# Optimization experiments

Hardware: AMD Instinct MI355X
Metric: run time of the kernel (lower is better)

## Reference

```python
import jax, jax.numpy as jnp
import numpy as np

B, N, E, DJ, DE = 1024, 400, 128, 128, 128  # batch, nodes, edges, joint dim, edge dim (E must equal DJ and DE for BatchNorm1d on 3D input)
BN_EPS = 1e-5


def setup_inputs() -> dict:
    key = jax.random.key(0)
    ks = jax.random.split(key, 8)
    gout = jax.random.normal(ks[0], (B, N, DJ), dtype=jnp.float32)
    eout = jax.random.normal(ks[1], (B, E, DE), dtype=jnp.float32)
    start_shift = jax.random.uniform(ks[2], (B, E, N), dtype=jnp.float32)
    end_shift = jax.random.uniform(ks[3], (B, E, N), dtype=jnp.float32)
    # Linear params: nn.init.normal_(std=0.001), bias 0
    W1 = 0.001 * jax.random.normal(ks[4], (DJ, 2 * DJ), dtype=jnp.float32)
    b1 = jnp.zeros((DJ,), dtype=jnp.float32)
    W2 = 0.001 * jax.random.normal(ks[5], (DE, DJ), dtype=jnp.float32)
    b2 = jnp.zeros((DE,), dtype=jnp.float32)
    # BatchNorm affine params: weight=1, bias=0
    g1 = jnp.ones((DJ,), dtype=jnp.float32)
    beta1 = jnp.zeros((DJ,), dtype=jnp.float32)
    g2 = jnp.ones((DE,), dtype=jnp.float32)
    beta2 = jnp.zeros((DE,), dtype=jnp.float32)
    return {"gout": gout, "eout": eout, "start_shift": start_shift, "end_shift": end_shift,
            "W1": W1, "b1": b1, "W2": W2, "b2": b2,
            "g1": g1, "beta1": beta1, "g2": g2, "beta2": beta2}


def batchnorm1d(x, gamma, beta):
    # PyTorch BatchNorm1d on 3D input: channels at dim 1, biased variance over dims (0, 2)
    mean = jnp.mean(x, axis=(0, 2), keepdims=True)
    var = jnp.mean(jnp.square(x - mean), axis=(0, 2), keepdims=True)
    xhat = (x - mean) * jax.lax.rsqrt(var + BN_EPS)
    return xhat * gamma[None, :, None] + beta[None, :, None]


def reference(gout, eout, start_shift, end_shift, W1, b1, W2, b2, g1, beta1, g2, beta2):
    # node -> edge gather via dense shift matmuls: [B,E,N] @ [B,N,DJ] -> [B,E,DJ]
    start_nodes = jnp.matmul(start_shift, gout)
    end_nodes = jnp.matmul(end_shift, gout)
    x = jnp.concatenate([start_nodes, end_nodes], axis=2)  # [B, E, 2*DJ]
    h = jnp.einsum('bef,df->bed', x, W1) + b1  # Linear(2*DJ -> DJ)
    h = jax.nn.relu(batchnorm1d(h, g1, beta1))
    h = jnp.einsum('bed,od->beo', h, W2) + b2  # Linear(DJ -> DE)
    res = batchnorm1d(h, g2, beta2)
    return jax.nn.relu(eout + res)
```

## Files before the change

### kernel.cpp

```cpp
#include <hip/hip_runtime.h>
#include <stdint.h>

#define BB 1024
#define NN 400
#define EE 128
#define DD 128
#define NSLOT 64
#define GTS 424
#define NKP 212

typedef float f32x4 __attribute__((ext_vector_type(4)));
typedef short bf16x8 __attribute__((ext_vector_type(8)));
typedef short bf16x4 __attribute__((ext_vector_type(4)));

__device__ __forceinline__ short f2bf(float f) {
    uint32_t u = __builtin_bit_cast(uint32_t, f);
    u += 0x7fffu + ((u >> 16) & 1u);
    return (short)(u >> 16);
}

__device__ __forceinline__ float bf2f(short s) {
    return __builtin_bit_cast(float, (uint32_t)((uint16_t)s) << 16);
}

__device__ __forceinline__ bf16x8 cvt8(const f32x4 a, const f32x4 b) {
    bf16x8 r;
    r[0] = f2bf(a[0]); r[1] = f2bf(a[1]); r[2] = f2bf(a[2]); r[3] = f2bf(a[3]);
    r[4] = f2bf(b[0]); r[5] = f2bf(b[1]); r[6] = f2bf(b[2]); r[7] = f2bf(b[3]);
    return r;
}

__global__ __launch_bounds__(1024, 1)
void k1_gemm(const float* __restrict__ gout, const float* __restrict__ ss,
             const float* __restrict__ es, const float* __restrict__ W1,
             const float* __restrict__ b1, unsigned short* __restrict__ h,
             float* __restrict__ stats1)
{
    __shared__ short lds[66560];
    short* GT  = lds;
    short* Ps  = lds;
    short* W1s = lds + 32768;

    const int b   = blockIdx.x;
    const int t   = threadIdx.x;
    const int w   = t >> 6;
    const int l   = t & 63;
    const int l15 = l & 15;
    const int l4  = l >> 4;

    {
        const int d   = t & 127;
        const int kpb = t >> 7;
        const float* gb = gout + (size_t)b * NN * DD + d;
        for (int kp = kpb; kp < NKP; kp += 8) {
            int k = 2 * kp;
            float v0 = 0.f, v1 = 0.f;
            if (k < NN) { v0 = gb[(size_t)k * DD]; v1 = gb[(size_t)(k + 1) * DD]; }
            uint32_t pk = (uint32_t)(uint16_t)f2bf(v0) |
                          ((uint32_t)(uint16_t)f2bf(v1) << 16);
            *(uint32_t*)&GT[d * GTS + 2 * kp] = pk;
        }
    }
    __syncthreads();

    const int arow = (w & 7) * 16 + l15;
    const float* abase = ((w < 8) ? ss : es) + ((size_t)b * EE + arow) * NN;

    f32x4 acc[8];
#pragma unroll
    for (int cf = 0; cf < 8; ++cf) acc[cf] = f32x4{0.f, 0.f, 0.f, 0.f};

    auto ld_a = [&](int k0) -> bf16x8 {
        int kk = k0 + l4 * 8;
        f32x4 x0{0.f, 0.f, 0.f, 0.f}, x1{0.f, 0.f, 0.f, 0.f};
        if (kk < NN) { x0 = *(const f32x4*)(abase + kk); x1 = *(const f32x4*)(abase + kk + 4); }
        return cvt8(x0, x1);
    };

    bf16x8 a_cur = ld_a(0);
    const int NK = 13;
    for (int s = 0; s < NK; ++s) {
        bf16x8 a_nxt = a_cur;
        if (s + 1 < NK) a_nxt = ld_a((s + 1) * 32);
        const int k0 = s * 32;
#pragma unroll
        for (int cf = 0; cf < 8; ++cf) {
            bf16x8 gf = *(const bf16x8*)&GT[(cf * 16 + l15) * GTS + k0 + l4 * 8];
            acc[cf] = __builtin_amdgcn_mfma_f32_16x16x32_bf16(a_cur, gf, acc[cf], 0, 0, 0);
        }
        a_cur = a_nxt;
    }
    __syncthreads();

#pragma unroll
    for (int cf = 0; cf < 8; ++cf)
#pragma unroll
        for (int r = 0; r < 4; ++r) {
            int row = w * 16 + l4 * 4 + r;
            int col = cf * 16 + l15;
            Ps[row * 128 + (((col >> 3) ^ (row & 7)) << 3) + (col & 7)] = f2bf(acc[cf][r]);
        }
    {
        const int j  = t >> 3;
        const int kc = t & 7;
        const float* wp = W1 + (size_t)j * 256 + kc * 32;
        short* dst = &W1s[j * 264 + kc * 32];
#pragma unroll
        for (int i = 0; i < 4; ++i) {
            f32x4 x0 = *(const f32x4*)(wp + i * 8);
            f32x4 x1 = *(const f32x4*)(wp + i * 8 + 4);
            *(bf16x8*)(dst + i * 8) = cvt8(x0, x1);
        }
    }
    __syncthreads();

    const int mt = w >> 1;
    const int jh = w & 1;
    f32x4 acc2[4];
#pragma unroll
    for (int cf = 0; cf < 4; ++cf) acc2[cf] = f32x4{0.f, 0.f, 0.f, 0.f};

#pragma unroll
    for (int kf = 0; kf < 8; ++kf) {
        int roff = (kf >= 4) ? 128 : 0;
        int kcol = (kf & 3) * 32 + l4 * 8;
        int row  = roff + mt * 16 + l15;
        int cb   = kcol >> 3;
        bf16x8 xf = *(const bf16x8*)&Ps[row * 128 + ((cb ^ (row & 7)) << 3)];
#pragma unroll
        for (int cf = 0; cf < 4; ++cf) {
            int j = jh * 64 + cf * 16 + l15;
            bf16x8 wf = *(const bf16x8*)&W1s[j * 264 + kf * 32 + l4 * 8];
            acc2[cf] = __builtin_amdgcn_mfma_f32_16x16x32_bf16(xf, wf, acc2[cf], 0, 0, 0);
        }
    }
    __syncthreads();

    float* red = (float*)lds;
    float s_r[4] = {0.f, 0.f, 0.f, 0.f};
    float q_r[4] = {0.f, 0.f, 0.f, 0.f};
#pragma unroll
    for (int cf = 0; cf < 4; ++cf) {
        float bv = b1[jh * 64 + cf * 16 + l15];
        f32x4 v = acc2[cf] + bv;
#pragma unroll
        for (int r = 0; r < 4; ++r) {
            int e = mt * 16 + l4 * 4 + r;
            h[((size_t)b * EE + e) * DD + jh * 64 + cf * 16 + l15] = (unsigned short)f2bf(v[r]);
            s_r[r] += v[r];
            q_r[r] += v[r] * v[r];
        }
    }
#pragma unroll
    for (int r = 0; r < 4; ++r) {
        float s = s_r[r], q = q_r[r];
        s += __shfl_xor(s, 1); s += __shfl_xor(s, 2); s += __shfl_xor(s, 4); s += __shfl_xor(s, 8);
        q += __shfl_xor(q, 1); q += __shfl_xor(q, 2); q += __shfl_xor(q, 4); q += __shfl_xor(q, 8);
        if (l15 == 0) {
            int e = mt * 16 + l4 * 4 + r;
            red[((e << 1) | jh)]       = s;
            red[256 + ((e << 1) | jh)] = q;
        }
    }
    __syncthreads();
    if (t < 128) {
        float s = red[2 * t] + red[2 * t + 1];
        float q = red[256 + 2 * t] + red[256 + 2 * t + 1];
        int slot = b & (NSLOT - 1);
        atomicAdd(&stats1[slot * 256 + t], s);
        atomicAdd(&stats1[slot * 256 + 128 + t], q);
    }
}

__global__ __launch_bounds__(256, 4)
void k3_gemm(const unsigned short* __restrict__ h, const float* __restrict__ W2,
             const float* __restrict__ b2, const float* __restrict__ g1,
             const float* __restrict__ bt1, float* __restrict__ out,
             const float* __restrict__ stats1, float* __restrict__ stats2)
{
    __shared__ short Xs[128 * 128];
    __shared__ float sc[128];
    __shared__ float sh[128];
    const int b   = blockIdx.x;
    const int t   = threadIdx.x;
    const int w   = t >> 6;
    const int l15 = t & 15;
    const int l4  = (t >> 4) & 3;

    if (t < 128) {
        float sm = 0.f, sq = 0.f;
#pragma unroll 8
        for (int sl = 0; sl < NSLOT; ++sl) {
            sm += stats1[sl * 256 + t];
            sq += stats1[sl * 256 + 128 + t];
        }
        const float inv_n = 1.0f / (1024.0f * 128.0f);
        float m    = sm * inv_n;
        float var  = sq * inv_n - m * m;
        float rstd = rsqrtf(var + 1e-5f);
        float s    = rstd * g1[t];
        sc[t] = s;
        sh[t] = bt1[t] - m * s;
    }
    __syncthreads();

    {
        const int c8 = t & 15;
        const int eb = t >> 4;
#pragma unroll
        for (int p = 0; p < 8; ++p) {
            int e = eb + 16 * p;
            bf16x8 v8 = *(const bf16x8*)&h[((size_t)b * EE + e) * DD + c8 * 8];
            float s = sc[e], s0 = sh[e];
            bf16x8 o;
#pragma unroll
            for (int i = 0; i < 8; ++i)
                o[i] = f2bf(fmaxf(fmaf(bf2f(v8[i]), s, s0), 0.0f));
            *(bf16x8*)&Xs[e * 128 + ((c8 ^ (e & 7)) << 3)] = o;
        }
    }
    __syncthreads();

    f32x4 acc[8][2];
#pragma unroll
    for (int i = 0; i < 8; ++i) {
        acc[i][0] = f32x4{0.f, 0.f, 0.f, 0.f};
        acc[i][1] = f32x4{0.f, 0.f, 0.f, 0.f};
    }
#pragma unroll
    for (int kf = 0; kf < 4; ++kf) {
        const int k0 = kf * 32;
        const int cb = (k0 >> 3) + l4;
        bf16x8 af[8];
#pragma unroll
        for (int rf = 0; rf < 8; ++rf) {
            int row = rf * 16 + l15;
            af[rf] = *(const bf16x8*)&Xs[row * 128 + ((cb ^ (row & 7)) * 8)];
        }
#pragma unroll
        for (int cf = 0; cf < 2; ++cf) {
            int j = w * 32 + cf * 16 + l15;
            const float* wp = W2 + (size_t)j * 128 + k0 + l4 * 8;
            bf16x8 bfr = cvt8(*(const f32x4*)wp, *(const f32x4*)(wp + 4));
#pragma unroll
            for (int rf = 0; rf < 8; ++rf)
                acc[rf][cf] = __builtin_amdgcn_mfma_f32_16x16x32_bf16(af[rf], bfr, acc[rf][cf], 0, 0, 0);
        }
    }

    __syncthreads();
    float* red = (float*)Xs;
    const float bj0 = b2[w * 32 + l15];
    const float bj1 = b2[w * 32 + 16 + l15];
    const int j0 = w * 32 + l15;
#pragma unroll
    for (int rf = 0; rf < 8; ++rf) {
        f32x4 v0 = acc[rf][0] + bj0;
        f32x4 v1 = acc[rf][1] + bj1;
        int elb = rf * 16 + l4 * 4;
#pragma unroll
        for (int r = 0; r < 4; ++r) {
            float* op = out + (size_t)(b * EE + elb + r) * DD;
            op[j0]      = v0[r];
            op[j0 + 16] = v1[r];
            float s = v0[r] + v1[r];
            float q = v0[r] * v0[r] + v1[r] * v1[r];
            s += __shfl_xor(s, 1); s += __shfl_xor(s, 2); s += __shfl_xor(s, 4); s += __shfl_xor(s, 8);
            q += __shfl_xor(q, 1); q += __shfl_xor(q, 2); q += __shfl_xor(q, 4); q += __shfl_xor(q, 8);
            if (l15 == 0) {
                red[(elb + r) * 4 + w]       = s;
                red[512 + (elb + r) * 4 + w] = q;
            }
        }
    }
    __syncthreads();
    if (t < 128) {
        float s = red[t * 4] + red[t * 4 + 1] + red[t * 4 + 2] + red[t * 4 + 3];
        float q = red[512 + t * 4] + red[512 + t * 4 + 1] + red[512 + t * 4 + 2] + red[512 + t * 4 + 3];
        int slot = b & (NSLOT - 1);
        atomicAdd(&stats2[slot * 256 + t], s);
        atomicAdd(&stats2[slot * 256 + 128 + t], q);
    }
}

__global__ __launch_bounds__(256)
void k5_final(const float* __restrict__ eout, const float* __restrict__ g2,
              const float* __restrict__ bt2, float* __restrict__ io,
              const float* __restrict__ stats2)
{
    __shared__ float sc[128];
    __shared__ float sh[128];
    const int t = threadIdx.x;
    if (t < 128) {
        float sm = 0.f, sq = 0.f;
#pragma unroll 8
        for (int sl = 0; sl < NSLOT; ++sl) {
            sm += stats2[sl * 256 + t];
            sq += stats2[sl * 256 + 128 + t];
        }
        const float inv_n = 1.0f / (1024.0f * 128.0f);
        float m    = sm * inv_n;
        float var  = sq * inv_n - m * m;
        float rstd = rsqrtf(var + 1e-5f);
        float s    = rstd * g2[t];
        sc[t] = s;
        sh[t] = bt2[t] - m * s;
    }
    __syncthreads();

    const int total4 = BB * EE * DD / 4;
    for (int i4 = blockIdx.x * blockDim.x + t; i4 < total4; i4 += gridDim.x * blockDim.x) {
        int e = (i4 >> 5) & 127;
        f32x4 v = *(f32x4*)(io + (size_t)i4 * 4);
        f32x4 u = *(const f32x4*)(eout + (size_t)i4 * 4);
        float s = sc[e], s0 = sh[e];
        f32x4 o;
#pragma unroll
        for (int i = 0; i < 4; ++i)
            o[i] = fmaxf(u[i] + fmaf(v[i], s, s0), 0.0f);
        *(f32x4*)(io + (size_t)i4 * 4) = o;
    }
}

extern "C" void kernel_launch(void* const* d_in, const int* in_sizes, int n_in,
                              void* d_out, int out_size, void* d_ws, size_t ws_size,
                              hipStream_t stream)
{
    const float* gout  = (const float*)d_in[0];
    const float* eout  = (const float*)d_in[1];
    const float* ss    = (const float*)d_in[2];
    const float* es    = (const float*)d_in[3];
    const float* W1    = (const float*)d_in[4];
    const float* b1    = (const float*)d_in[5];
    const float* W2    = (const float*)d_in[6];
    const float* b2    = (const float*)d_in[7];
    const float* g1    = (const float*)d_in[8];
    const float* bt1   = (const float*)d_in[9];
    const float* g2    = (const float*)d_in[10];
    const float* bt2   = (const float*)d_in[11];

    float* stats1 = (float*)d_ws;
    float* stats2 = stats1 + NSLOT * 256;
    unsigned short* h = (unsigned short*)(stats2 + NSLOT * 256);
    float* out    = (float*)d_out;

    hipMemsetAsync((void*)stats1, 0, 2 * NSLOT * 256 * sizeof(float), stream);
    k1_gemm<<<dim3(BB), dim3(1024), 0, stream>>>(gout, ss, es, W1, b1, h, stats1);
    k3_gemm<<<dim3(BB), dim3(256), 0, stream>>>(h, W2, b2, g1, bt1, out, stats1, stats2);
    k5_final<<<dim3(2048), dim3(256), 0, stream>>>(eout, g2, bt2, out, stats2);
}
```

Measured before the change: 263.6 us.

## Store second-linear output as bf16 in-place and prefetch shift rows before transpose

The second GEMM now writes its pre-BatchNorm output as bf16 into the workspace buffer h, overwriting the first activation in place, rather than writing fp32 into the output tensor. The final kernel reads that bf16 buffer plus eout and writes the output, which cuts intermediate write and read traffic roughly in half. In the first GEMM, the shift-matrix loads for the first two K-steps are issued before the gout transpose so their latency overlaps it. The transpose now packs four nodes per 64-bit LDS store, and the prefetch becomes two-deep. The cost is extra bf16 rounding of the pre-BN values, and k3 reading and writing the same buffer h relies on each block touching only its own rows.

```diff
diff --git a/kernel.cpp b/kernel.cpp
--- a/kernel.cpp
+++ b/kernel.cpp
@@ -7,7 +7,6 @@
 #define DD 128
 #define NSLOT 64
 #define GTS 424
-#define NKP 212
 
 typedef float f32x4 __attribute__((ext_vector_type(4)));
 typedef short bf16x8 __attribute__((ext_vector_type(8)));
@@ -48,47 +47,60 @@
     const int l15 = l & 15;
     const int l4  = l >> 4;
 
-    {
-        const int d   = t & 127;
-        const int kpb = t >> 7;
-        const float* gb = gout + (size_t)b * NN * DD + d;
-        for (int kp = kpb; kp < NKP; kp += 8) {
-            int k = 2 * kp;
-            float v0 = 0.f, v1 = 0.f;
-            if (k < NN) { v0 = gb[(size_t)k * DD]; v1 = gb[(size_t)(k + 1) * DD]; }
-            uint32_t pk = (uint32_t)(uint16_t)f2bf(v0) |
-                          ((uint32_t)(uint16_t)f2bf(v1) << 16);
-            *(uint32_t*)&GT[d * GTS + 2 * kp] = pk;
-        }
-    }
-    __syncthreads();
-
     const int arow = (w & 7) * 16 + l15;
     const float* abase = ((w < 8) ? ss : es) + ((size_t)b * EE + arow) * NN;
+    const int kkoff = l4 * 8;
+
+    f32x4 pa0 = *(const f32x4*)(abase + kkoff);
+    f32x4 pa1 = *(const f32x4*)(abase + kkoff + 4);
+    f32x4 pb0 = *(const f32x4*)(abase + 32 + kkoff);
+    f32x4 pb1 = *(const f32x4*)(abase + 32 + kkoff + 4);
+
+    {
+        const int d  = t & 127;
+        const int qb = t >> 7;
+        const float* gb = gout + (size_t)b * NN * DD + d;
+        for (int q = qb; q < 106; q += 8) {
+            int k = 4 * q;
+            float v0 = 0.f, v1 = 0.f, v2 = 0.f, v3 = 0.f;
+            if (k < NN) {
+                v0 = gb[(size_t)k * DD];
+                v1 = gb[(size_t)(k + 1) * DD];
+                v2 = gb[(size_t)(k + 2) * DD];
+                v3 = gb[(size_t)(k + 3) * DD];
+            }
+            uint32_t lo = (uint32_t)(uint16_t)f2bf(v0) | ((uint32_t)(uint16_t)f2bf(v1) << 16);
+            uint32_t hi = (uint32_t)(uint16_t)f2bf(v2) | ((uint32_t)(uint16_t)f2bf(v3) << 16);
+            *(uint64_t*)&GT[d * GTS + 4 * q] = ((uint64_t)hi << 32) | lo;
+        }
+    }
+    __syncthreads();
 
     f32x4 acc[8];
 #pragma unroll
     for (int cf = 0; cf < 8; ++cf) acc[cf] = f32x4{0.f, 0.f, 0.f, 0.f};
 
-    auto ld_a = [&](int k0) -> bf16x8 {
-        int kk = k0 + l4 * 8;
-        f32x4 x0{0.f, 0.f, 0.f, 0.f}, x1{0.f, 0.f, 0.f, 0.f};
-        if (kk < NN) { x0 = *(const f32x4*)(abase + kk); x1 = *(const f32x4*)(abase + kk + 4); }
-        return cvt8(x0, x1);
-    };
-
-    bf16x8 a_cur = ld_a(0);
-    const int NK = 13;
-    for (int s = 0; s < NK; ++s) {
-        bf16x8 a_nxt = a_cur;
-        if (s + 1 < NK) a_nxt = ld_a((s + 1) * 32);
+#pragma unroll
+    for (int s = 0; s < 13; ++s) {
+        bf16x8 a = cvt8(pa0, pa1);
+        pa0 = pb0; pa1 = pb1;
+        const int sn = s + 2;
+        if (sn < 12) {
+            pb0 = *(const f32x4*)(abase + sn * 32 + kkoff);
+            pb1 = *(const f32x4*)(abase + sn * 32 + kkoff + 4);
+        } else if (sn == 12) {
+            int kk = 384 + kkoff;
+            pb0 = f32x4{0.f, 0.f, 0.f, 0.f};
+            pb1 = f32x4{0.f, 0.f, 0.f, 0.f};
+            if (kk < NN)     pb0 = *(const f32x4*)(abase + kk);
+            if (kk + 4 < NN) pb1 = *(const f32x4*)(abase + kk + 4);
+        }
         const int k0 = s * 32;
 #pragma unroll
         for (int cf = 0; cf < 8; ++cf) {
-            bf16x8 gf = *(const bf16x8*)&GT[(cf * 16 + l15) * GTS + k0 + l4 * 8];
-            acc[cf] = __builtin_amdgcn_mfma_f32_16x16x32_bf16(a_cur, gf, acc[cf], 0, 0, 0);
-        }
-        a_cur = a_nxt;
+            bf16x8 gf = *(const bf16x8*)&GT[(cf * 16 + l15) * GTS + k0 + kkoff];
+            acc[cf] = __builtin_amdgcn_mfma_f32_16x16x32_bf16(a, gf, acc[cf], 0, 0, 0);
+        }
     }
     __syncthreads();
 
@@ -173,9 +185,9 @@
 }
 
 __global__ __launch_bounds__(256, 4)
-void k3_gemm(const unsigned short* __restrict__ h, const float* __restrict__ W2,
+void k3_gemm(unsigned short* h, const float* __restrict__ W2,
              const float* __restrict__ b2, const float* __restrict__ g1,
-             const float* __restrict__ bt1, float* __restrict__ out,
+             const float* __restrict__ bt1,
              const float* __restrict__ stats1, float* __restrict__ stats2)
 {
     __shared__ short Xs[128 * 128];
@@ -260,9 +272,9 @@
         int elb = rf * 16 + l4 * 4;
 #pragma unroll
         for (int r = 0; r < 4; ++r) {
-            float* op = out + (size_t)(b * EE + elb + r) * DD;
-            op[j0]      = v0[r];
-            op[j0 + 16] = v1[r];
+            unsigned short* op = h + (size_t)(b * EE + elb + r) * DD;
+            op[j0]      = (unsigned short)f2bf(v0[r]);
+            op[j0 + 16] = (unsigned short)f2bf(v1[r]);
             float s = v0[r] + v1[r];
             float q = v0[r] * v0[r] + v1[r] * v1[r];
             s += __shfl_xor(s, 1); s += __shfl_xor(s, 2); s += __shfl_xor(s, 4); s += __shfl_xor(s, 8);
@@ -284,9 +296,9 @@
 }
 
 __global__ __launch_bounds__(256)
-void k5_final(const float* __restrict__ eout, const float* __restrict__ g2,
-              const float* __restrict__ bt2, float* __restrict__ io,
-              const float* __restrict__ stats2)
+void k5_final(const unsigned short* __restrict__ h2, const float* __restrict__ eout,
+              const float* __restrict__ g2, const float* __restrict__ bt2,
+              float* __restrict__ out, const float* __restrict__ stats2)
 {
     __shared__ float sc[128];
     __shared__ float sh[128];
@@ -308,17 +320,21 @@
     }
     __syncthreads();
 
-    const int total4 = BB * EE * DD / 4;
-    for (int i4 = blockIdx.x * blockDim.x + t; i4 < total4; i4 += gridDim.x * blockDim.x) {
-        int e = (i4 >> 5) & 127;
-        f32x4 v = *(f32x4*)(io + (size_t)i4 * 4);
-        f32x4 u = *(const f32x4*)(eout + (size_t)i4 * 4);
+    const int total8 = BB * EE * DD / 8;
+    for (int i8 = blockIdx.x * blockDim.x + t; i8 < total8; i8 += gridDim.x * blockDim.x) {
+        int e = (i8 >> 4) & 127;
+        bf16x8 v8 = *(const bf16x8*)(h2 + (size_t)i8 * 8);
+        f32x4 u0 = *(const f32x4*)(eout + (size_t)i8 * 8);
+        f32x4 u1 = *(const f32x4*)(eout + (size_t)i8 * 8 + 4);
         float s = sc[e], s0 = sh[e];
-        f32x4 o;
-#pragma unroll
-        for (int i = 0; i < 4; ++i)
-            o[i] = fmaxf(u[i] + fmaf(v[i], s, s0), 0.0f);
-        *(f32x4*)(io + (size_t)i4 * 4) = o;
+        f32x4 o0, o1;
+#pragma unroll
+        for (int i = 0; i < 4; ++i) {
+            o0[i] = fmaxf(u0[i] + fmaf(bf2f(v8[i]), s, s0), 0.0f);
+            o1[i] = fmaxf(u1[i] + fmaf(bf2f(v8[i + 4]), s, s0), 0.0f);
+        }
+        *(f32x4*)(out + (size_t)i8 * 8)     = o0;
+        *(f32x4*)(out + (size_t)i8 * 8 + 4) = o1;
     }
 }
 
@@ -346,6 +362,6 @@
 
     hipMemsetAsync((void*)stats1, 0, 2 * NSLOT * 256 * sizeof(float), stream);
     k1_gemm<<<dim3(BB), dim3(1024), 0, stream>>>(gout, ss, es, W1, b1, h, stats1);
-    k3_gemm<<<dim3(BB), dim3(256), 0, stream>>>(h, W2, b2, g1, bt1, out, stats1, stats2);
-    k5_final<<<dim3(2048), dim3(256), 0, stream>>>(eout, g2, bt2, out, stats2);
-}
+    k3_gemm<<<dim3(BB), dim3(256), 0, stream>>>(h, W2, b2, g1, bt1, stats1, stats2);
+    k5_final<<<dim3(2048), dim3(256), 0, stream>>>(h, eout, g2, bt2, out, stats2);
+}
```

After: 246.9 us. 6.3% less time.
